# Optimization experiments

Hardware: AMD Instinct MI355X
Metric: run time of the kernel (lower is better)

Reference implementation:

```python
import jax, jax.numpy as jnp
import numpy as np

B = 16384          # number of positions (segments)
TOT = 491520       # total active features per color (~30 per position)
NF = 768           # 2*6*64 feature space


def setup_inputs() -> dict:
    key = jax.random.key(0)
    ks = jax.random.split(key, 10)
    white_features = jax.random.randint(ks[0], (TOT,), 0, NF)
    white_indices = jnp.sort(jax.random.randint(ks[1], (TOT,), 0, B)).at[-1].set(B - 1)
    black_features = jax.random.randint(ks[2], (TOT,), 0, NF)
    black_indices = jnp.sort(jax.random.randint(ks[3], (TOT,), 0, B)).at[-1].set(B - 1)
    W1 = jax.random.normal(ks[4], (64, NF), dtype=jnp.float32) * 0.05
    b1 = jax.random.normal(ks[5], (64,), dtype=jnp.float32) * 0.05
    W2 = jax.random.normal(ks[6], (32, 128), dtype=jnp.float32) * 0.05
    b2 = jax.random.normal(ks[7], (32,), dtype=jnp.float32) * 0.05
    W3 = jax.random.normal(ks[8], (1, 32), dtype=jnp.float32) * 0.05
    b3 = jax.random.normal(ks[9], (1,), dtype=jnp.float32) * 0.05
    return {
        "white_features": white_features, "white_indices": white_indices,
        "black_features": black_features, "black_indices": black_indices,
        "W1": W1, "b1": b1, "W2": W2, "b2": b2, "W3": W3, "b3": b3,
        "num_segments": B,
    }


def reference(white_features, white_indices, black_features, black_indices,
              W1, b1, W2, b2, W3, b3, num_segments):
    W1T = W1.T  # [NF, 64]

    def feed_l1(feats, idx):
        f = jnp.take(W1T, feats, axis=0)                       # [TOT, 64] gather
        a = jax.ops.segment_sum(f, idx, num_segments=num_segments)  # [B, 64]
        return a + b1

    a1w = feed_l1(white_features, white_indices)
    a1b = feed_l1(black_features, black_indices)
    a1 = jnp.clip(jnp.concatenate([a1w, a1b], axis=1), 0.0, 1.0)  # hardtanh(0,1)
    a2 = jnp.clip(a1 @ W2.T + b2, 0.0, 1.0)
    a3 = jax.nn.sigmoid(a2 @ W3.T + b3)
    return a3.squeeze(-1)
```

## Files before the change

kernel.cpp:

```cpp
#include <hip/hip_runtime.h>
#include <hip/hip_fp16.h>
#include <math.h>

#define NPOS 16384
#define NTOT 491520
#define NFEAT 768
#define DUMMY 768
#define PITCH 68

typedef _Float16 h2 __attribute__((ext_vector_type(2)));

__device__ __forceinline__ int imin(int a, int b) { return a < b ? a : b; }
__device__ __forceinline__ float clamp01(float x) { return fminf(fmaxf(x, 0.f), 1.f); }

#if __has_builtin(__builtin_amdgcn_fdot2)
#define FDOT2(a, b, c) __builtin_amdgcn_fdot2((a), (b), (c), false)
#else
#define FDOT2(a, b, c) ((c) + (float)(a)[0] * (float)(b)[0] + (float)(a)[1] * (float)(b)[1])
#endif

__device__ __forceinline__ h2 toh2(__half2 x) { return __builtin_bit_cast(h2, x); }

__global__ __launch_bounds__(1024, 4) void k_all(
    const int* __restrict__ wf, const int* __restrict__ bf,
    const int* __restrict__ wi, const int* __restrict__ bi,
    const float* __restrict__ W1, const float4* __restrict__ b1q,
    const float* __restrict__ W2, const float* __restrict__ b2,
    const float* __restrict__ W3, const float* __restrict__ b3,
    float* __restrict__ out)
{
    __shared__ __half  w1t[769 * PITCH];
    __shared__ __half2 w2t[2048];
    __shared__ int     ivs[16][64];
    __shared__ uint4   a1sq[16][16];
    __shared__ int     sb[2][65];

    int t = threadIdx.x;
    int wave = t >> 6, lane = t & 63;
    int p0 = blockIdx.x * 64;

    if (wave < 14) {
        int r = lane;
        for (int i = 0; ; ++i) {
            int f4 = wave + 14 * i;
            if (f4 >= 192) break;
            float4 v = *(const float4*)&W1[r * NFEAT + f4 * 4];
            int fb = f4 * 4;
            w1t[(fb + 0) * PITCH + r] = __float2half(v.x);
            w1t[(fb + 1) * PITCH + r] = __float2half(v.y);
            w1t[(fb + 2) * PITCH + r] = __float2half(v.z);
            w1t[(fb + 3) * PITCH + r] = __float2half(v.w);
        }
        for (int x = t; x < 2048; x += 896) {
            int i = x >> 5, j = x & 31;
            w2t[x] = __floats2half2_rn(W2[j * 128 + 2 * i], W2[j * 128 + 2 * i + 1]);
        }
        if (t < 64) w1t[DUMMY * PITCH + t] = __float2half(0.f);
    } else {
        const int* arr = (wave == 14) ? wi : bi;
        int col = wave - 14;
        int tgt1 = p0 + lane, tgt2 = p0 + 64;
        int lo1 = 0, hi1 = NTOT, lo2 = 0, hi2 = NTOT;
        while (lo1 < hi1 || lo2 < hi2) {
            if (lo1 < hi1) {
                int m = (lo1 + hi1) >> 1;
                if (arr[m] < tgt1) lo1 = m + 1; else hi1 = m;
            }
            if (lo2 < hi2) {
                int m = (lo2 + hi2) >> 1;
                if (arr[m] < tgt2) lo2 = m + 1; else hi2 = m;
            }
        }
        sb[col][lane] = lo1;
        if (lane == 63) sb[col][64] = lo2;
    }
    __syncthreads();

    int g = lane >> 4, k = lane & 15;
    int j = lane & 31, h = lane >> 5;

    h2 w2r[32];
#pragma unroll
    for (int i = 0; i < 32; ++i) w2r[i] = toh2(w2t[(h * 32 + i) * 32 + j]);

    float4 bb = b1q[k];
    float b2j = b2[j], w3j = W3[j], b30 = b3[0];

    int* myiv = &ivs[wave][0];
    __half2* a1h = (__half2*)&a1sq[wave][0];

    for (int it = 0; it < 4; ++it) {
        int pl = wave + 16 * it;
        int pos = p0 + pl;
        int ws_ = sb[0][pl], we = sb[0][pl + 1];
        int bs_ = sb[1][pl], be = sb[1][pl + 1];

        float wa0 = 0.f, wa1 = 0.f, wa2 = 0.f, wa3 = 0.f;
        float ba0 = 0.f, ba1 = 0.f, ba2 = 0.f, ba3 = 0.f;

        auto run = [&](const int* __restrict__ feats, int s, int e,
                       float& A0, float& A1, float& A2, float& A3) {
            for (int tt = s; tt < e; tt += 64) {
                myiv[lane] = (tt + lane < e) ? feats[tt + lane] : DUMMY;
                int nc = (imin(e - tt, 64) + 15) >> 4;
                for (int c = 0; c < nc; ++c) {
                    int base = c * 16 + g;
                    int f0 = myiv[base];
                    int f1 = myiv[base + 4];
                    int f2 = myiv[base + 8];
                    int f3 = myiv[base + 12];
                    uint2 d0 = *(const uint2*)&w1t[f0 * PITCH + k * 4];
                    uint2 d1 = *(const uint2*)&w1t[f1 * PITCH + k * 4];
                    uint2 d2 = *(const uint2*)&w1t[f2 * PITCH + k * 4];
                    uint2 d3 = *(const uint2*)&w1t[f3 * PITCH + k * 4];
                    h2 l0 = __builtin_bit_cast(h2, d0.x), u0 = __builtin_bit_cast(h2, d0.y);
                    h2 l1 = __builtin_bit_cast(h2, d1.x), u1 = __builtin_bit_cast(h2, d1.y);
                    h2 l2 = __builtin_bit_cast(h2, d2.x), u2 = __builtin_bit_cast(h2, d2.y);
                    h2 l3 = __builtin_bit_cast(h2, d3.x), u3 = __builtin_bit_cast(h2, d3.y);
                    A0 += (float)l0[0] + (float)l1[0] + (float)l2[0] + (float)l3[0];
                    A1 += (float)l0[1] + (float)l1[1] + (float)l2[1] + (float)l3[1];
                    A2 += (float)u0[0] + (float)u1[0] + (float)u2[0] + (float)u3[0];
                    A3 += (float)u0[1] + (float)u1[1] + (float)u2[1] + (float)u3[1];
                }
            }
        };
        run(wf, ws_, we, wa0, wa1, wa2, wa3);
        run(bf, bs_, be, ba0, ba1, ba2, ba3);

        wa0 += __shfl_xor(wa0, 16); wa0 += __shfl_xor(wa0, 32);
        wa1 += __shfl_xor(wa1, 16); wa1 += __shfl_xor(wa1, 32);
        wa2 += __shfl_xor(wa2, 16); wa2 += __shfl_xor(wa2, 32);
        wa3 += __shfl_xor(wa3, 16); wa3 += __shfl_xor(wa3, 32);
        ba0 += __shfl_xor(ba0, 16); ba0 += __shfl_xor(ba0, 32);
        ba1 += __shfl_xor(ba1, 16); ba1 += __shfl_xor(ba1, 32);
        ba2 += __shfl_xor(ba2, 16); ba2 += __shfl_xor(ba2, 32);
        ba3 += __shfl_xor(ba3, 16); ba3 += __shfl_xor(ba3, 32);

        if (lane < 32) {
            __half2 q0, q1;
            if (g == 0) {
                q0 = __floats2half2_rn(clamp01(wa0 + bb.x), clamp01(wa1 + bb.y));
                q1 = __floats2half2_rn(clamp01(wa2 + bb.z), clamp01(wa3 + bb.w));
            } else {
                q0 = __floats2half2_rn(clamp01(ba0 + bb.x), clamp01(ba1 + bb.y));
                q1 = __floats2half2_rn(clamp01(ba2 + bb.z), clamp01(ba3 + bb.w));
            }
            a1h[g * 32 + k * 2]     = q0;
            a1h[g * 32 + k * 2 + 1] = q1;
        }

        const uint4* aq = &a1sq[wave][h * 8];
        float acc = 0.f;
#pragma unroll
        for (int q4 = 0; q4 < 8; ++q4) {
            uint4 qq = aq[q4];
            acc = FDOT2(__builtin_bit_cast(h2, qq.x), w2r[q4 * 4 + 0], acc);
            acc = FDOT2(__builtin_bit_cast(h2, qq.y), w2r[q4 * 4 + 1], acc);
            acc = FDOT2(__builtin_bit_cast(h2, qq.z), w2r[q4 * 4 + 2], acc);
            acc = FDOT2(__builtin_bit_cast(h2, qq.w), w2r[q4 * 4 + 3], acc);
        }
        acc += __shfl_xor(acc, 32);

        float a2v = clamp01(acc + b2j);
        float p = a2v * w3j;
        p += __shfl_xor(p, 16);
        p += __shfl_xor(p, 8);
        p += __shfl_xor(p, 4);
        p += __shfl_xor(p, 2);
        p += __shfl_xor(p, 1);
        if (lane == 0)
            out[pos] = 1.f / (1.f + __expf(-(p + b30)));
    }
}

extern "C" void kernel_launch(void* const* d_in, const int* in_sizes, int n_in,
                              void* d_out, int out_size, void* d_ws, size_t ws_size,
                              hipStream_t stream) {
    const int*   wf = (const int*)d_in[0];
    const int*   wi = (const int*)d_in[1];
    const int*   bf = (const int*)d_in[2];
    const int*   bi = (const int*)d_in[3];
    const float* W1 = (const float*)d_in[4];
    const float* b1 = (const float*)d_in[5];
    const float* W2 = (const float*)d_in[6];
    const float* b2 = (const float*)d_in[7];
    const float* W3 = (const float*)d_in[8];
    const float* b3 = (const float*)d_in[9];
    float* out = (float*)d_out;

    k_all<<<NPOS / 64, 1024, 0, stream>>>(wf, bf, wi, bi, W1, (const float4*)b1,
                                          W2, b2, W3, b3, out);
}
```

Measured before the change: 26.66 us.

## Use interpolation search for segment bounds and rebalance setup work across waves

Replaces the plain binary search over the sorted index arrays with an interpolation search that guesses about 30 entries per position, then falls back to bisection, which should cut the number of dependent global loads during setup. W2 transposition and the dummy-row zeroing move from the W1-loading waves to the two search waves. The feature-index reads in the accumulation loop become one 16-byte shared load per group instead of four scalar loads. The interpolation guess assumes a roughly uniform feature count per position, and the extra work on the search waves may lengthen their part of the setup.

```diff
diff --git a/kernel.cpp b/kernel.cpp
--- a/kernel.cpp
+++ b/kernel.cpp
@@ -31,7 +31,7 @@
 {
     __shared__ __half  w1t[769 * PITCH];
     __shared__ __half2 w2t[2048];
-    __shared__ int     ivs[16][64];
+    __shared__ __align__(16) int ivs[16][64];
     __shared__ uint4   a1sq[16][16];
     __shared__ int     sb[2][65];
 
@@ -41,38 +41,66 @@
 
     if (wave < 14) {
         int r = lane;
-        for (int i = 0; ; ++i) {
+        const float* wrow = W1 + r * NFEAT;
+#pragma unroll 2
+        for (int i = 0; i < 14; ++i) {
             int f4 = wave + 14 * i;
             if (f4 >= 192) break;
-            float4 v = *(const float4*)&W1[r * NFEAT + f4 * 4];
+            float4 v = *(const float4*)&wrow[f4 * 4];
             int fb = f4 * 4;
             w1t[(fb + 0) * PITCH + r] = __float2half(v.x);
             w1t[(fb + 1) * PITCH + r] = __float2half(v.y);
             w1t[(fb + 2) * PITCH + r] = __float2half(v.z);
             w1t[(fb + 3) * PITCH + r] = __float2half(v.w);
         }
-        for (int x = t; x < 2048; x += 896) {
-            int i = x >> 5, j = x & 31;
-            w2t[x] = __floats2half2_rn(W2[j * 128 + 2 * i], W2[j * 128 + 2 * i + 1]);
-        }
-        if (t < 64) w1t[DUMMY * PITCH + t] = __float2half(0.f);
     } else {
-        const int* arr = (wave == 14) ? wi : bi;
+        const int* __restrict__ arr = (wave == 14) ? wi : bi;
         int col = wave - 14;
-        int tgt1 = p0 + lane, tgt2 = p0 + 64;
-        int lo1 = 0, hi1 = NTOT, lo2 = 0, hi2 = NTOT;
-        while (lo1 < hi1 || lo2 < hi2) {
-            if (lo1 < hi1) {
-                int m = (lo1 + hi1) >> 1;
-                if (arr[m] < tgt1) lo1 = m + 1; else hi1 = m;
-            }
-            if (lo2 < hi2) {
-                int m = (lo2 + hi2) >> 1;
-                if (arr[m] < tgt2) lo2 = m + 1; else hi2 = m;
-            }
+        int t1 = p0 + lane, t2 = p0 + 64;
+        int lo1 = 0, hi1 = 0, g1 = 0;
+        int lo2 = 0, hi2 = 0, g2 = 0;
+        if (t1 > 0) { hi1 = NTOT; g1 = imin(t1 * 30, NTOT - 1); }
+        if (t2 < NPOS) { hi2 = NTOT; g2 = imin(t2 * 30, NTOT - 1); }
+        else { lo2 = NTOT; hi2 = NTOT; }
+#pragma unroll 1
+        for (int it = 0; it < 8; ++it) {
+            bool c1 = lo1 < hi1, c2 = lo2 < hi2;
+            if (!c1 && !c2) break;
+            int v1 = 0, v2 = 0;
+            if (c1) v1 = arr[g1];
+            if (c2) v2 = arr[g2];
+            if (c1) {
+                if (v1 < t1) lo1 = g1 + 1; else hi1 = g1;
+                int ng = g1 + (t1 - v1) * 30;
+                if (ng < lo1 || ng >= hi1) ng = lo1 + ((hi1 - lo1) >> 1);
+                g1 = ng;
+            }
+            if (c2) {
+                if (v2 < t2) lo2 = g2 + 1; else hi2 = g2;
+                int ng = g2 + (t2 - v2) * 30;
+                if (ng < lo2 || ng >= hi2) ng = lo2 + ((hi2 - lo2) >> 1);
+                g2 = ng;
+            }
+        }
+#pragma unroll 1
+        for (;;) {
+            bool c1 = lo1 < hi1, c2 = lo2 < hi2;
+            if (!c1 && !c2) break;
+            int m1 = 0, m2 = 0, v1 = 0, v2 = 0;
+            if (c1) { m1 = lo1 + ((hi1 - lo1) >> 1); v1 = arr[m1]; }
+            if (c2) { m2 = lo2 + ((hi2 - lo2) >> 1); v2 = arr[m2]; }
+            if (c1) { if (v1 < t1) lo1 = m1 + 1; else hi1 = m1; }
+            if (c2) { if (v2 < t2) lo2 = m2 + 1; else hi2 = m2; }
         }
         sb[col][lane] = lo1;
         if (lane == 63) sb[col][64] = lo2;
+
+        int tl = t - 896;
+        for (int x = tl; x < 2048; x += 128) {
+            int i = x >> 5, jj = x & 31;
+            w2t[x] = __floats2half2_rn(W2[jj * 128 + 2 * i], W2[jj * 128 + 2 * i + 1]);
+        }
+        if (tl < 64) w1t[DUMMY * PITCH + tl] = __float2half(0.f);
     }
     __syncthreads();
 
@@ -104,15 +132,11 @@
                 myiv[lane] = (tt + lane < e) ? feats[tt + lane] : DUMMY;
                 int nc = (imin(e - tt, 64) + 15) >> 4;
                 for (int c = 0; c < nc; ++c) {
-                    int base = c * 16 + g;
-                    int f0 = myiv[base];
-                    int f1 = myiv[base + 4];
-                    int f2 = myiv[base + 8];
-                    int f3 = myiv[base + 12];
-                    uint2 d0 = *(const uint2*)&w1t[f0 * PITCH + k * 4];
-                    uint2 d1 = *(const uint2*)&w1t[f1 * PITCH + k * 4];
-                    uint2 d2 = *(const uint2*)&w1t[f2 * PITCH + k * 4];
-                    uint2 d3 = *(const uint2*)&w1t[f3 * PITCH + k * 4];
+                    uint4 iq = *(const uint4*)&myiv[c * 16 + g * 4];
+                    uint2 d0 = *(const uint2*)&w1t[(int)iq.x * PITCH + k * 4];
+                    uint2 d1 = *(const uint2*)&w1t[(int)iq.y * PITCH + k * 4];
+                    uint2 d2 = *(const uint2*)&w1t[(int)iq.z * PITCH + k * 4];
+                    uint2 d3 = *(const uint2*)&w1t[(int)iq.w * PITCH + k * 4];
                     h2 l0 = __builtin_bit_cast(h2, d0.x), u0 = __builtin_bit_cast(h2, d0.y);
                     h2 l1 = __builtin_bit_cast(h2, d1.x), u1 = __builtin_bit_cast(h2, d1.y);
                     h2 l2 = __builtin_bit_cast(h2, d2.x), u2 = __builtin_bit_cast(h2, d2.y);
```

New measurement: 27.42 us. 1.03x slower.
